# Performance work log

Measured on AMD Instinct MI355X. Metric: run time of the kernel, lower is better.

## Reference

```python
import jax, jax.numpy as jnp
import numpy as np

ALPHA = 1.0

def setup_inputs() -> dict:
    key = jax.random.key(0)
    k1, k2 = jax.random.split(key)
    x = jax.random.normal(k1, (65536, 512), dtype=jnp.float32)
    clusters = jax.random.normal(k2, (1024, 512), dtype=jnp.float32)
    return {"x": x, "clusters": clusters}

def reference(x, clusters):
    # same math as sum((x[:,None,:]-c)^2, -1) without the [N,K,D] intermediate)
    x_sq = jnp.sum(x * x, axis=1, keepdims=True)          # [N,1]
    c_sq = jnp.sum(clusters * clusters, axis=1)           # [K]
    cross = x @ clusters.T                                # [N,K]
    dist2 = jnp.maximum(x_sq + c_sq[None, :] - 2.0 * cross, 0.0)
    q = 1.0 / (1.0 + dist2 / ALPHA)
    q = q ** ((ALPHA + 1.0) / 2.0)
    q = q / jnp.sum(q, axis=1, keepdims=True)             # row-normalize
    return q
```

## Files before the change

### kernel.cpp

```cpp
#include <hip/hip_runtime.h>
#include <stdint.h>
#include <stddef.h>

#define DDIM   512
#define KCL    1024
#define BK     32
#define KSTEPS (DDIM / BK)
#define RPB    64
#define THR    512
#define NROWS  65536
#define NBLK   (NROWS / RPB)

#define SB_BYTES   (KCL * BK * 2)
#define SA_STRIDE  40
#define SA_BYTES   (RPB * SA_STRIDE * 2)
#define SMEM_BYTES (2 * SB_BYTES + 2 * SA_BYTES + 512)

typedef __attribute__((ext_vector_type(4))) float    floatx4;
typedef __attribute__((ext_vector_type(8))) _Float16 half8;
typedef __attribute__((ext_vector_type(4))) _Float16 half4;

__device__ __forceinline__ void gload_lds16(const void* g, void* l) {
    __builtin_amdgcn_global_load_lds(
        (const __attribute__((address_space(1))) unsigned char*)g,
        (__attribute__((address_space(3))) unsigned char*)l,
        16, 0, 0);
}

__global__ __launch_bounds__(256) void prep_kernel(const float* __restrict__ clusters,
                                                   _Float16* __restrict__ wsB,
                                                   float* __restrict__ csq) {
    const int l  = threadIdx.x & 63;
    const int c  = (blockIdx.x << 2) + (threadIdx.x >> 6);
    const int ks = l >> 2;
    const int j  = l & 3;

    const float* src = clusters + (size_t)c * DDIM + ks * BK + j * 8;
    floatx4 f0 = *(const floatx4*)src;
    floatx4 f1 = *(const floatx4*)(src + 4);

    half8 h;
    h[0] = (_Float16)f0[0]; h[1] = (_Float16)f0[1]; h[2] = (_Float16)f0[2]; h[3] = (_Float16)f0[3];
    h[4] = (_Float16)f1[0]; h[5] = (_Float16)f1[1]; h[6] = (_Float16)f1[2]; h[7] = (_Float16)f1[3];

    const int p = (j + (c >> 1)) & 3;
    *(half8*)(wsB + (size_t)ks * (KCL * BK) + c * BK + p * 8) = h;

    float ss = f0[0]*f0[0] + f0[1]*f0[1] + f0[2]*f0[2] + f0[3]*f0[3]
             + f1[0]*f1[0] + f1[1]*f1[1] + f1[2]*f1[2] + f1[3]*f1[3];
    ss += __shfl_xor(ss, 1,  64);
    ss += __shfl_xor(ss, 2,  64);
    ss += __shfl_xor(ss, 4,  64);
    ss += __shfl_xor(ss, 8,  64);
    ss += __shfl_xor(ss, 16, 64);
    ss += __shfl_xor(ss, 32, 64);
    if (l == 0) csq[c] = ss;
}

__global__ __launch_bounds__(THR, 2)
void cluster_kernel(const float* __restrict__ x,
                    const _Float16* __restrict__ wsB,
                    const float* __restrict__ csq,
                    float* __restrict__ out) {
    extern __shared__ char smem[];
    char* const sB0 = smem;
    char* const sB1 = smem + SB_BYTES;
    char* const sA0 = smem + 2 * SB_BYTES;
    char* const sA1 = smem + 2 * SB_BYTES + SA_BYTES;
    float* const xsq    = (float*)(smem + 2 * SB_BYTES + 2 * SA_BYTES);
    float* const rowsum = (float*)(smem + 2 * SB_BYTES + 2 * SA_BYTES + 256);

    const int t      = threadIdx.x;
    const int l      = t & 63;
    const int w      = t >> 6;
    const int lane16 = l & 15;
    const int kgrp   = l >> 4;
    const int row0   = blockIdx.x * RPB;
    const int wcol   = w << 7;

    if (t < 64) { xsq[t] = 0.f; rowsum[t] = 0.f; }
    __syncthreads();

    int aoff[4];
#pragma unroll
    for (int rt = 0; rt < 4; ++rt)
        aoff[rt] = (rt * 16 + lane16) * (SA_STRIDE * 2) + kgrp * 16;
    int boff[8];
#pragma unroll
    for (int ct = 0; ct < 8; ++ct) {
        const int c = wcol + ct * 16 + lane16;
        const int p = (kgrp + (c >> 1)) & 3;
        boff[ct] = c * 64 + p * 16;
    }

    const int ar = t >> 3;
    const int ac = (t & 7) << 2;
    const float* const aptr = x + (size_t)(row0 + ar) * DDIM + ac;
    const int awoff = ar * (SA_STRIDE * 2) + ac * 2;

    floatx4 acc[4][8];
#pragma unroll
    for (int rt = 0; rt < 4; ++rt)
#pragma unroll
        for (int ct = 0; ct < 8; ++ct)
            acc[rt][ct] = (floatx4){0.f, 0.f, 0.f, 0.f};

    {
        floatx4 f = __builtin_nontemporal_load((const floatx4*)aptr);
#pragma unroll
        for (int it = 0; it < 8; ++it) {
            const int ch = it * THR + t;
            gload_lds16(wsB + ch * 8, sB0 + ch * 16);
        }
        half4 h;
        h[0] = (_Float16)f[0]; h[1] = (_Float16)f[1]; h[2] = (_Float16)f[2]; h[3] = (_Float16)f[3];
        *(half4*)(sA0 + awoff) = h;
        float ss = f[0]*f[0] + f[1]*f[1] + f[2]*f[2] + f[3]*f[3];
        ss += __shfl_xor(ss, 1, 64);
        ss += __shfl_xor(ss, 2, 64);
        ss += __shfl_xor(ss, 4, 64);
        if ((t & 7) == 0) atomicAdd(&xsq[ar], ss);
    }

#pragma unroll 2
    for (int k = 0; k < KSTEPS; ++k) {
        char* const sBb = (k & 1) ? sB1 : sB0;
        char* const sAb = (k & 1) ? sA1 : sA0;
        char* const sBn = (k & 1) ? sB0 : sB1;
        char* const sAn = (k & 1) ? sA0 : sA1;

        __syncthreads();

        floatx4 f;
        const bool more = (k + 1 < KSTEPS);
        if (more) {
            f = __builtin_nontemporal_load((const floatx4*)(aptr + (k + 1) * BK));
            const _Float16* wb = wsB + (size_t)(k + 1) * (KCL * BK);
#pragma unroll
            for (int it = 0; it < 8; ++it) {
                const int ch = it * THR + t;
                gload_lds16(wb + ch * 8, sBn + ch * 16);
            }
        }

        half8 aF[4];
#pragma unroll
        for (int rt = 0; rt < 4; ++rt)
            aF[rt] = *(const half8*)(sAb + aoff[rt]);
#pragma unroll
        for (int ct = 0; ct < 8; ++ct) {
            const half8 bF = *(const half8*)(sBb + boff[ct]);
#pragma unroll
            for (int rt = 0; rt < 4; ++rt)
                acc[rt][ct] = __builtin_amdgcn_mfma_f32_16x16x32_f16(aF[rt], bF, acc[rt][ct], 0, 0, 0);
        }

        if (more) {
            half4 h;
            h[0] = (_Float16)f[0]; h[1] = (_Float16)f[1]; h[2] = (_Float16)f[2]; h[3] = (_Float16)f[3];
            *(half4*)(sAn + awoff) = h;
            float ss = f[0]*f[0] + f[1]*f[1] + f[2]*f[2] + f[3]*f[3];
            ss += __shfl_xor(ss, 1, 64);
            ss += __shfl_xor(ss, 2, 64);
            ss += __shfl_xor(ss, 4, 64);
            if ((t & 7) == 0) atomicAdd(&xsq[ar], ss);
        }
    }

    float cs[8];
#pragma unroll
    for (int ct = 0; ct < 8; ++ct)
        cs[ct] = csq[wcol + ct * 16 + lane16];
    floatx4 xv[4];
#pragma unroll
    for (int rt = 0; rt < 4; ++rt)
        xv[rt] = *(const floatx4*)(xsq + rt * 16 + kgrp * 4);

    float rp[4][4];
#pragma unroll
    for (int rt = 0; rt < 4; ++rt) {
#pragma unroll
        for (int i = 0; i < 4; ++i) {
            const float xr = xv[rt][i];
            float s = 0.f;
#pragma unroll
            for (int ct = 0; ct < 8; ++ct) {
                float d = xr + cs[ct] - 2.0f * acc[rt][ct][i];
                d = fmaxf(d, 0.0f);
                const float q = __builtin_amdgcn_rcpf(1.0f + d);
                acc[rt][ct][i] = q;
                s += q;
            }
            rp[rt][i] = s;
        }
    }
#pragma unroll
    for (int m = 1; m <= 8; m <<= 1)
#pragma unroll
        for (int rt = 0; rt < 4; ++rt)
#pragma unroll
            for (int i = 0; i < 4; ++i)
                rp[rt][i] += __shfl_xor(rp[rt][i], m, 64);
    if (lane16 == 0) {
#pragma unroll
        for (int rt = 0; rt < 4; ++rt)
#pragma unroll
            for (int i = 0; i < 4; ++i)
                atomicAdd(&rowsum[rt * 16 + kgrp * 4 + i], rp[rt][i]);
    }
    __syncthreads();

#pragma unroll
    for (int rt = 0; rt < 4; ++rt) {
        const floatx4 rs = *(const floatx4*)(rowsum + rt * 16 + kgrp * 4);
#pragma unroll
        for (int i = 0; i < 4; ++i) {
            const float inv = __builtin_amdgcn_rcpf(rs[i]);
            float* orow = out + (size_t)(row0 + rt * 16 + kgrp * 4 + i) * KCL + wcol + lane16;
#pragma unroll
            for (int ct = 0; ct < 8; ++ct)
                __builtin_nontemporal_store(acc[rt][ct][i] * inv, orow + ct * 16);
        }
    }
}

extern "C" void kernel_launch(void* const* d_in, const int* in_sizes, int n_in,
                              void* d_out, int out_size, void* d_ws, size_t ws_size,
                              hipStream_t stream) {
    (void)in_sizes; (void)n_in; (void)out_size; (void)ws_size;
    const float* x        = (const float*)d_in[0];
    const float* clusters = (const float*)d_in[1];
    float* out = (float*)d_out;

    _Float16* wsB = (_Float16*)d_ws;
    float*    csq = (float*)((char*)d_ws + (size_t)KSTEPS * KCL * BK * 2);

    hipFuncSetAttribute((const void*)cluster_kernel,
                        hipFuncAttributeMaxDynamicSharedMemorySize, SMEM_BYTES);

    prep_kernel<<<KCL / 4, 256, 0, stream>>>(clusters, wsB, csq);
    cluster_kernel<<<NBLK, THR, SMEM_BYTES, stream>>>(x, wsB, csq, out);
}
```

Measured before the change: 460.6 us.

## Double threads per block to 16 waves, halving per-wave column tile

Raises the block size from 512 to 1024 threads. Each of the 16 waves now covers 64 cluster columns instead of 128, so the accumulator tile shrinks from 4x8 to 4x4 MFMA tiles and A/B staging is redistributed across more threads with 2-float loads. The goal is more waves per CU to hide LDS and global latency, and lower register pressure. The per-wave ratio of MFMA work to A-fragment LDS reads drops, and output stores switch from nontemporal to regular stores.

After: 443.4 us. -3.7%, faster.

```diff
diff --git a/kernel.cpp b/kernel.cpp
--- a/kernel.cpp
+++ b/kernel.cpp
@@ -7,7 +7,7 @@
 #define BK     32
 #define KSTEPS (DDIM / BK)
 #define RPB    64
-#define THR    512
+#define THR    1024
 #define NROWS  65536
 #define NBLK   (NROWS / RPB)
 
@@ -17,8 +17,9 @@
 #define SMEM_BYTES (2 * SB_BYTES + 2 * SA_BYTES + 512)
 
 typedef __attribute__((ext_vector_type(4))) float    floatx4;
+typedef __attribute__((ext_vector_type(2))) float    floatx2;
 typedef __attribute__((ext_vector_type(8))) _Float16 half8;
-typedef __attribute__((ext_vector_type(4))) _Float16 half4;
+typedef __attribute__((ext_vector_type(2))) _Float16 half2v;
 
 __device__ __forceinline__ void gload_lds16(const void* g, void* l) {
     __builtin_amdgcn_global_load_lds(
@@ -57,7 +58,7 @@
     if (l == 0) csq[c] = ss;
 }
 
-__global__ __launch_bounds__(THR, 2)
+__global__ __launch_bounds__(THR, 4)
 void cluster_kernel(const float* __restrict__ x,
                     const _Float16* __restrict__ wsB,
                     const float* __restrict__ csq,
@@ -76,50 +77,44 @@
     const int lane16 = l & 15;
     const int kgrp   = l >> 4;
     const int row0   = blockIdx.x * RPB;
-    const int wcol   = w << 7;
+    const int wcol   = w << 6;
 
     if (t < 64) { xsq[t] = 0.f; rowsum[t] = 0.f; }
     __syncthreads();
 
-    int aoff[4];
-#pragma unroll
-    for (int rt = 0; rt < 4; ++rt)
-        aoff[rt] = (rt * 16 + lane16) * (SA_STRIDE * 2) + kgrp * 16;
-    int boff[8];
-#pragma unroll
-    for (int ct = 0; ct < 8; ++ct) {
-        const int c = wcol + ct * 16 + lane16;
-        const int p = (kgrp + (c >> 1)) & 3;
-        boff[ct] = c * 64 + p * 16;
-    }
-
-    const int ar = t >> 3;
-    const int ac = (t & 7) << 2;
+    const int abase = lane16 * (SA_STRIDE * 2) + kgrp * 16;
+    const int c0    = wcol + lane16;
+    const int p0    = (kgrp + (c0 >> 1)) & 3;
+    const int bbase = c0 * 64 + p0 * 16;
+
+    const int ar = t >> 4;
+    const int ac = (t & 15) << 1;
     const float* const aptr = x + (size_t)(row0 + ar) * DDIM + ac;
     const int awoff = ar * (SA_STRIDE * 2) + ac * 2;
 
-    floatx4 acc[4][8];
+    floatx4 acc[4][4];
 #pragma unroll
     for (int rt = 0; rt < 4; ++rt)
 #pragma unroll
-        for (int ct = 0; ct < 8; ++ct)
+        for (int ct = 0; ct < 4; ++ct)
             acc[rt][ct] = (floatx4){0.f, 0.f, 0.f, 0.f};
 
     {
-        floatx4 f = __builtin_nontemporal_load((const floatx4*)aptr);
-#pragma unroll
-        for (int it = 0; it < 8; ++it) {
+        floatx2 f = __builtin_nontemporal_load((const floatx2*)aptr);
+#pragma unroll
+        for (int it = 0; it < 4; ++it) {
             const int ch = it * THR + t;
             gload_lds16(wsB + ch * 8, sB0 + ch * 16);
         }
-        half4 h;
-        h[0] = (_Float16)f[0]; h[1] = (_Float16)f[1]; h[2] = (_Float16)f[2]; h[3] = (_Float16)f[3];
-        *(half4*)(sA0 + awoff) = h;
-        float ss = f[0]*f[0] + f[1]*f[1] + f[2]*f[2] + f[3]*f[3];
+        half2v h;
+        h[0] = (_Float16)f[0]; h[1] = (_Float16)f[1];
+        *(half2v*)(sA0 + awoff) = h;
+        float ss = f[0]*f[0] + f[1]*f[1];
         ss += __shfl_xor(ss, 1, 64);
         ss += __shfl_xor(ss, 2, 64);
         ss += __shfl_xor(ss, 4, 64);
-        if ((t & 7) == 0) atomicAdd(&xsq[ar], ss);
+        ss += __shfl_xor(ss, 8, 64);
+        if ((t & 15) == 0) atomicAdd(&xsq[ar], ss);
     }
 
 #pragma unroll 2
@@ -131,13 +126,13 @@
 
         __syncthreads();
 
-        floatx4 f;
+        floatx2 f;
         const bool more = (k + 1 < KSTEPS);
         if (more) {
-            f = __builtin_nontemporal_load((const floatx4*)(aptr + (k + 1) * BK));
+            f = __builtin_nontemporal_load((const floatx2*)(aptr + (k + 1) * BK));
             const _Float16* wb = wsB + (size_t)(k + 1) * (KCL * BK);
 #pragma unroll
-            for (int it = 0; it < 8; ++it) {
+            for (int it = 0; it < 4; ++it) {
                 const int ch = it * THR + t;
                 gload_lds16(wb + ch * 8, sBn + ch * 16);
             }
@@ -146,30 +141,31 @@
         half8 aF[4];
 #pragma unroll
         for (int rt = 0; rt < 4; ++rt)
-            aF[rt] = *(const half8*)(sAb + aoff[rt]);
-#pragma unroll
-        for (int ct = 0; ct < 8; ++ct) {
-            const half8 bF = *(const half8*)(sBb + boff[ct]);
+            aF[rt] = *(const half8*)(sAb + abase + rt * (16 * SA_STRIDE * 2));
+#pragma unroll
+        for (int ct = 0; ct < 4; ++ct) {
+            const half8 bF = *(const half8*)(sBb + bbase + ct * 1024);
 #pragma unroll
             for (int rt = 0; rt < 4; ++rt)
                 acc[rt][ct] = __builtin_amdgcn_mfma_f32_16x16x32_f16(aF[rt], bF, acc[rt][ct], 0, 0, 0);
         }
 
         if (more) {
-            half4 h;
-            h[0] = (_Float16)f[0]; h[1] = (_Float16)f[1]; h[2] = (_Float16)f[2]; h[3] = (_Float16)f[3];
-            *(half4*)(sAn + awoff) = h;
-            float ss = f[0]*f[0] + f[1]*f[1] + f[2]*f[2] + f[3]*f[3];
+            half2v h;
+            h[0] = (_Float16)f[0]; h[1] = (_Float16)f[1];
+            *(half2v*)(sAn + awoff) = h;
+            float ss = f[0]*f[0] + f[1]*f[1];
             ss += __shfl_xor(ss, 1, 64);
             ss += __shfl_xor(ss, 2, 64);
             ss += __shfl_xor(ss, 4, 64);
-            if ((t & 7) == 0) atomicAdd(&xsq[ar], ss);
-        }
-    }
-
-    float cs[8];
-#pragma unroll
-    for (int ct = 0; ct < 8; ++ct)
+            ss += __shfl_xor(ss, 8, 64);
+            if ((t & 15) == 0) atomicAdd(&xsq[ar], ss);
+        }
+    }
+
+    float cs[4];
+#pragma unroll
+    for (int ct = 0; ct < 4; ++ct)
         cs[ct] = csq[wcol + ct * 16 + lane16];
     floatx4 xv[4];
 #pragma unroll
@@ -184,7 +180,7 @@
             const float xr = xv[rt][i];
             float s = 0.f;
 #pragma unroll
-            for (int ct = 0; ct < 8; ++ct) {
+            for (int ct = 0; ct < 4; ++ct) {
                 float d = xr + cs[ct] - 2.0f * acc[rt][ct][i];
                 d = fmaxf(d, 0.0f);
                 const float q = __builtin_amdgcn_rcpf(1.0f + d);
@@ -218,8 +214,8 @@
             const float inv = __builtin_amdgcn_rcpf(rs[i]);
             float* orow = out + (size_t)(row0 + rt * 16 + kgrp * 4 + i) * KCL + wcol + lane16;
 #pragma unroll
-            for (int ct = 0; ct < 8; ++ct)
-                __builtin_nontemporal_store(acc[rt][ct][i] * inv, orow + ct * 16);
+            for (int ct = 0; ct < 4; ++ct)
+                orow[ct * 16] = acc[rt][ct][i] * inv;
         }
     }
 }
```
